# Kernel tuning notes

Measured on AMD Instinct MI355X. Metric: run time of the kernel, lower is better.

The kernel has to match this reference:

```python
import jax, jax.numpy as jnp
import numpy as np

N_NODES = 100000
N_EDGES = 1600000
IN_DIM = 128
HID_DIM = 32
OUT_DIM = 64
N_REL = 8
N_CLASSES = 2


def setup_inputs() -> dict:
    key = jax.random.key(0)
    ks = jax.random.split(key, 12)
    x = jax.random.normal(ks[0], (N_NODES, IN_DIM), dtype=jnp.float32)
    edge_index = jax.random.randint(ks[1], (2, N_EDGES), 0, N_NODES, dtype=jnp.int64)
    edge_type = jax.random.randint(ks[2], (N_EDGES,), 0, N_REL, dtype=jnp.int64)
    # FastRGCNConv params: per-relation weight W [R, in, out], root weight, bias
    def glorot(k, shape):
        fan_in, fan_out = shape[-2], shape[-1]
        s = jnp.sqrt(6.0 / (fan_in + fan_out))
        return jax.random.uniform(k, shape, jnp.float32, -s, s)
    W1 = glorot(ks[3], (N_REL, IN_DIM, HID_DIM))
    root1 = glorot(ks[4], (IN_DIM, HID_DIM))
    b1 = jnp.zeros((HID_DIM,), jnp.float32)
    W2 = glorot(ks[5], (N_REL, HID_DIM, OUT_DIM))
    root2 = glorot(ks[6], (HID_DIM, OUT_DIM))
    b2 = jnp.zeros((OUT_DIM,), jnp.float32)
    lin_w = glorot(ks[7], (OUT_DIM, N_CLASSES))
    lin_b = jnp.zeros((N_CLASSES,), jnp.float32)
    return {"x": x, "edge_index": edge_index, "edge_type": edge_type,
            "W1": W1, "root1": root1, "b1": b1,
            "W2": W2, "root2": root2, "b2": b2,
            "lin_w": lin_w, "lin_b": lin_b}


def _fast_rgcn_conv(x, W, root, b, src, dst, etype, n_nodes):
    """FastRGCNConv: per-relation transform, gather by (src, relation),
    mean-aggregate by destination, plus root transform and bias."""
    # Transform all nodes by all relation weights: [N, R, H]
    xW = jnp.einsum('nf,rfh->nrh', x, W)
    # Per-edge message: relation-specific transformed source feature [E, H]
    msg = xW[src, etype]
    agg = jax.ops.segment_sum(msg, dst, num_segments=n_nodes)
    deg = jax.ops.segment_sum(jnp.ones((src.shape[0],), x.dtype), dst,
                              num_segments=n_nodes)
    agg = agg / jnp.maximum(deg, 1.0)[:, None]  # mean aggregation
    return agg + x @ root + b


def reference(x, edge_index, edge_type, W1, root1, b1, W2, root2, b2, lin_w, lin_b):
    src, dst = edge_index[0], edge_index[1]
    n = x.shape[0]
    h = jax.nn.relu(_fast_rgcn_conv(x, W1, root1, b1, src, dst, edge_type, n))
    h = _fast_rgcn_conv(h, W2, root2, b2, src, dst, edge_type, n)
    return h @ lin_w + lin_b
```

## Files before the change

kernel.cpp:

```cpp
#include <hip/hip_runtime.h>

#define NN      100000
#define IN_DIM  128
#define HID     32
#define ODIM    64
#define L1C     288
#define L2K     288
#define NWGS    196
#define NCB     784
#define CCAP    40
#define RECCAP  2304
#define G2ST    296

using bf16x8 = __attribute__((ext_vector_type(8))) short;
using f32x4  = __attribute__((ext_vector_type(4))) float;

__device__ __forceinline__ float bf2f(short s) {
    unsigned int u = ((unsigned int)(unsigned short)s) << 16;
    float f; __builtin_memcpy(&f, &u, 4); return f;
}
__device__ __forceinline__ short f2bf(float f) {
    unsigned int u; __builtin_memcpy(&u, &f, 4);
    u += 0x7fffu + ((u >> 16) & 1u);
    return (short)(u >> 16);
}
__device__ __forceinline__ float ldf(const void* p, int i, int f32) {
    return f32 ? ((const float*)p)[i] : bf2f(((const short*)p)[i]);
}
__device__ __forceinline__ int ldi(const int* p, long long i, int i64) {
    return i64 ? p[2 * i] : p[(int)i];
}

__global__ __launch_bounds__(256) void detect(const short* __restrict__ x,
                                              const short* __restrict__ W1,
                                              const short* __restrict__ r1,
                                              const short* __restrict__ W2,
                                              const short* __restrict__ r2,
                                              const short* __restrict__ lw,
                                              const int* __restrict__ ei,
                                              const int* __restrict__ et,
                                              int* __restrict__ flags) {
    __shared__ int cnt[8];
    if (threadIdx.x < 8) cnt[threadIdx.x] = 0;
    __syncthreads();
    const short* ptrs[6] = {x, W1, r1, W2, r2, lw};
    const int    nsmp[6] = {2048, 2048, 2048, 2048, 1024, 64};
    for (int j = 0; j < 6; ++j) {
        int w = 0;
        for (int i = threadIdx.x; i < nsmp[j]; i += 256) {
            unsigned int s = (unsigned short)ptrs[j][2 * i];
            unsigned int e = (s >> 7) & 0xFF;
            if (e >= 140u || (e >= 1u && e <= 100u)) w++;
        }
        if (w) atomicAdd(&cnt[j], w);
    }
    int wi = 0, wt = 0;
    if (threadIdx.x < 128) {
        if (ei[2 * threadIdx.x + 1] != 0) wi = 1;
        if (et[2 * threadIdx.x + 1] != 0) wt = 1;
    }
    if (wi) atomicAdd(&cnt[6], 1);
    if (wt) atomicAdd(&cnt[7], 1);
    __syncthreads();
    if (threadIdx.x == 0) {
        const int ns[6] = {2048, 2048, 2048, 2048, 1024, 64};
        for (int j = 0; j < 6; ++j) flags[j] = (cnt[j] * 4 > ns[j]) ? 1 : 0;
        flags[6] = (cnt[6] == 0) ? 1 : 0;
        flags[7] = (cnt[7] == 0) ? 1 : 0;
    }
}

__global__ __launch_bounds__(256) void prep_w1(const void* __restrict__ W1,
                                               const void* __restrict__ root1,
                                               short* __restrict__ w1t,
                                               const int* __restrict__ flags) {
    int i = blockIdx.x * 256 + threadIdx.x;
    if (i >= L1C * IN_DIM) return;
    int c = i >> 7, f = i & 127;
    float v;
    if (c < 256) { int r = c >> 5, h = c & 31; v = ldf(W1, (r * IN_DIM + f) * HID + h, flags[1]); }
    else         { v = ldf(root1, f * HID + (c - 256), flags[2]); }
    w1t[c * IN_DIM + f] = f2bf(v);
}
__global__ __launch_bounds__(256) void prep_w2c(const void* __restrict__ W2,
                                                const void* __restrict__ root2,
                                                short* __restrict__ w2ct,
                                                const int* __restrict__ flags) {
    int i = blockIdx.x * 256 + threadIdx.x;
    if (i >= ODIM * L2K) return;
    int c = i / L2K, k = i % L2K;
    float v;
    if (k < 256) { int r = k >> 5, kk = k & 31; v = ldf(W2, (r * HID + kk) * ODIM + c, flags[3]); }
    else         { v = ldf(root2, (k - 256) * ODIM + c, flags[4]); }
    w2ct[c * L2K + k] = f2bf(v);
}
__global__ __launch_bounds__(256) void prep_small(const short* __restrict__ b1,
                                                  const short* __restrict__ b2,
                                                  const void* __restrict__ lin_w,
                                                  const short* __restrict__ lin_b,
                                                  short* __restrict__ smallc,
                                                  const int* __restrict__ flags) {
    int i = threadIdx.x;
    if (i < 32)        smallc[i] = b1[i];
    else if (i < 96)   smallc[i] = b2[i - 32];
    else if (i < 224)  smallc[i] = f2bf(ldf(lin_w, i - 96, flags[5]));
    else if (i < 226)  smallc[i] = lin_b[i - 224];
}

__global__ __launch_bounds__(1024) void scatter_coarse(const int* __restrict__ ei,
                                                       const int* __restrict__ et,
                                                       int* __restrict__ cnt,
                                                       int* __restrict__ seg, int E,
                                                       const int* __restrict__ flags) {
    __shared__ int cur[NCB];
    if (threadIdx.x < NCB) cur[threadIdx.x] = 0;
    __syncthreads();
    int i64 = flags[6], t64 = flags[7];
    int epw = (E + NWGS - 1) / NWGS;
    int lo = blockIdx.x * epw;
    int hi = lo + epw; if (hi > E) hi = E;
    for (int i = lo + threadIdx.x; i < hi; i += 1024) {
        int s = ldi(ei, i, i64);
        int d = ldi(ei, (long long)E + i, i64);
        int r = ldi(et, i, t64);
        int cb = d >> 7;
        int pos = atomicAdd(&cur[cb], 1);
        if (pos < CCAP)
            seg[(cb * NWGS + (int)blockIdx.x) * CCAP + pos] = ((d & 127) << 20) | (s << 3) | r;
    }
    __syncthreads();
    if (threadIdx.x < NCB) {
        int c = cur[threadIdx.x];
        cnt[blockIdx.x * NCB + threadIdx.x] = c < CCAP ? c : CCAP;
    }
}

__global__ __launch_bounds__(64) void cb_sum(const int* __restrict__ cnt,
                                             int* __restrict__ cbTot) {
    int cb = blockIdx.x, lane = threadIdx.x;
    int t = 0;
    for (int g = lane; g < NWGS; g += 64) t += cnt[g * NCB + cb];
#pragma unroll
    for (int o = 32; o > 0; o >>= 1) t += __shfl_down(t, o, 64);
    if (lane == 0) cbTot[cb] = t;
}

__global__ __launch_bounds__(1024) void cb_scan2(const int* __restrict__ cbTot,
                                                 int* __restrict__ cbBase,
                                                 int* __restrict__ off) {
    __shared__ int s[1024];
    int t = threadIdx.x;
    int v = (t < NCB) ? cbTot[t] : 0;
    s[t] = v; __syncthreads();
    for (int o = 1; o < 1024; o <<= 1) {
        int u = (t >= o) ? s[t - o] : 0;
        __syncthreads();
        s[t] += u;
        __syncthreads();
    }
    if (t < NCB) cbBase[t] = s[t] - v;
    if (t == NCB - 1) off[NN] = s[t];
}

__global__ __launch_bounds__(256) void build_cb(const int* __restrict__ cnt,
                                                const int* __restrict__ seg,
                                                const int* __restrict__ cbBase,
                                                int* __restrict__ off,
                                                float* __restrict__ inv_deg,
                                                int* __restrict__ packed) {
    __shared__ int cntl[NWGS], soff[NWGS];
    __shared__ int recs[RECCAP];
    __shared__ int degl[128], basel[128], kcur[128];
    __shared__ int stmp[256];
    int cb = blockIdx.x, tid = threadIdx.x;
    if (tid < NWGS) cntl[tid] = cnt[tid * NCB + cb];
    if (tid < 128) degl[tid] = 0;
    __syncthreads();
    int v = (tid < NWGS) ? cntl[tid] : 0;
    stmp[tid] = v; __syncthreads();
    for (int o = 1; o < 256; o <<= 1) {
        int u = (tid >= o) ? stmp[tid - o] : 0;
        __syncthreads();
        stmp[tid] += u;
        __syncthreads();
    }
    if (tid < NWGS) soff[tid] = stmp[tid] - v;
    int tot = stmp[255]; if (tot > RECCAP) tot = RECCAP;
    __syncthreads();
    int wave = tid >> 6, lane = tid & 63;
    for (int g = wave; g < NWGS; g += 4) {
        int c = cntl[g], b = soff[g];
        const int* sp = seg + (cb * NWGS + g) * CCAP;
        for (int e = lane; e < c; e += 64)
            if (b + e < RECCAP) recs[b + e] = sp[e];
    }
    __syncthreads();
    for (int i = tid; i < tot; i += 256) atomicAdd(&degl[recs[i] >> 20], 1);
    __syncthreads();
    int dv = (tid < 128) ? degl[tid] : 0;
    stmp[tid] = dv; __syncthreads();
    for (int o = 1; o < 128; o <<= 1) {
        int u = (tid >= o) ? stmp[tid - o] : 0;
        __syncthreads();
        stmp[tid] += u;
        __syncthreads();
    }
    int gbase = cbBase[cb];
    if (tid < 128) {
        int excl = stmp[tid] - dv;
        basel[tid] = excl;
        kcur[tid] = 0;
        int node = cb * 128 + tid;
        if (node < NN) {
            off[node] = gbase + excl;
            inv_deg[node] = 1.0f / (float)(dv > 1 ? dv : 1);
        }
    }
    __syncthreads();
    for (int i = tid; i < tot; i += 256) {
        int rec = recs[i];
        int n = rec >> 20;
        int p = atomicAdd(&kcur[n], 1);
        packed[gbase + basel[n] + p] = rec & 0xFFFFF;
    }
}

__global__ __launch_bounds__(256) void gemm1(const void* __restrict__ x,
                                             const short* __restrict__ w1t,
                                             short* __restrict__ xw,
                                             const int* __restrict__ flags) {
    int wave = threadIdx.x >> 6, lane = threadIdx.x & 63;
    int m = lane & 15, quad = lane >> 4;
    int row0 = (blockIdx.x * 4 + wave) * 64;
    if (row0 >= NN) return;

    bf16x8 a[4][4];
    int fp32 = flags[0];
#pragma unroll
    for (int t = 0; t < 4; ++t) {
        int row = row0 + t * 16 + m;
        int rc = row < NN ? row : NN - 1;
        if (fp32) {
            const float* xr = (const float*)x + rc * IN_DIM + quad * 8;
#pragma unroll
            for (int kt = 0; kt < 4; ++kt) {
                const f32x4* q = (const f32x4*)(xr + kt * 32);
                f32x4 u0 = q[0], u1 = q[1];
                bf16x8 tt;
                tt[0] = f2bf(u0[0]); tt[1] = f2bf(u0[1]); tt[2] = f2bf(u0[2]); tt[3] = f2bf(u0[3]);
                tt[4] = f2bf(u1[0]); tt[5] = f2bf(u1[1]); tt[6] = f2bf(u1[2]); tt[7] = f2bf(u1[3]);
                a[t][kt] = tt;
            }
        } else {
            const short* xr = (const short*)x + rc * IN_DIM + quad * 8;
#pragma unroll
            for (int kt = 0; kt < 4; ++kt) a[t][kt] = *(const bf16x8*)(xr + kt * 32);
        }
    }

    for (int ct = 0; ct < 18; ++ct) {
        const short* wp = w1t + (ct * 16 + m) * IN_DIM + quad * 8;
        bf16x8 b[4];
#pragma unroll
        for (int kt = 0; kt < 4; ++kt) b[kt] = *(const bf16x8*)(wp + kt * 32);
#pragma unroll
        for (int t = 0; t < 4; ++t) {
            f32x4 acc = {0.f, 0.f, 0.f, 0.f};
#pragma unroll
            for (int kt = 0; kt < 4; ++kt)
                acc = __builtin_amdgcn_mfma_f32_16x16x32_bf16(a[t][kt], b[kt], acc, 0, 0, 0);
#pragma unroll
            for (int i = 0; i < 4; ++i) {
                int r = row0 + t * 16 + quad * 4 + i;
                if (r < NN) xw[r * L1C + ct * 16 + m] = f2bf(acc[i]);
            }
        }
    }
}

__global__ __launch_bounds__(256) void agg1(const short* __restrict__ xw,
                                            const int* __restrict__ off,
                                            const int* __restrict__ packed,
                                            const float* __restrict__ inv_deg,
                                            const short* __restrict__ smallc,
                                            short* __restrict__ h) {
    int lane = threadIdx.x & 31;
    int node = blockIdx.x * 8 + (threadIdx.x >> 5);
    if (node >= NN) return;
    int s = off[node], e = off[node + 1];
    float acc = 0.f;
    int i = s;
    for (; i + 3 < e; i += 4) {
        int pk0 = packed[i], pk1 = packed[i + 1], pk2 = packed[i + 2], pk3 = packed[i + 3];
        float v0 = bf2f(xw[(pk0 >> 3) * L1C + (pk0 & 7) * 32 + lane]);
        float v1 = bf2f(xw[(pk1 >> 3) * L1C + (pk1 & 7) * 32 + lane]);
        float v2 = bf2f(xw[(pk2 >> 3) * L1C + (pk2 & 7) * 32 + lane]);
        float v3 = bf2f(xw[(pk3 >> 3) * L1C + (pk3 & 7) * 32 + lane]);
        acc += (v0 + v1) + (v2 + v3);
    }
    for (; i < e; ++i) {
        int pk = packed[i];
        acc += bf2f(xw[(pk >> 3) * L1C + (pk & 7) * 32 + lane]);
    }
    float v = acc * inv_deg[node] + bf2f(xw[node * L1C + 256 + lane]) + bf2f(smallc[lane]);
    h[node * HID + lane] = f2bf(v > 0.f ? v : 0.f);
}

__global__ __launch_bounds__(256) void agg2_fused(const short* __restrict__ h,
                                                  const int* __restrict__ off,
                                                  const int* __restrict__ packed,
                                                  const float* __restrict__ inv_deg,
                                                  const short* __restrict__ w2ct,
                                                  const short* __restrict__ smallc,
                                                  float* __restrict__ out) {
    __shared__ __align__(16) short g2l[16 * G2ST];
    __shared__ float red[4][16][2];
    int tid = threadIdx.x;
    int lane31 = tid & 31, gi = tid >> 5;
    int row0 = blockIdx.x * 16;

    for (int s2 = 0; s2 < 2; ++s2) {
        int n = row0 + gi * 2 + s2;
        int st = off[n], e = off[n + 1];
        float a0 = 0, a1 = 0, a2 = 0, a3 = 0, a4 = 0, a5 = 0, a6 = 0, a7 = 0;
        int i = st;
        for (; i + 3 < e; i += 4) {
            int pk0 = packed[i], pk1 = packed[i + 1], pk2 = packed[i + 2], pk3 = packed[i + 3];
            float v0 = bf2f(h[(pk0 >> 3) * HID + lane31]);
            float v1 = bf2f(h[(pk1 >> 3) * HID + lane31]);
            float v2 = bf2f(h[(pk2 >> 3) * HID + lane31]);
            float v3 = bf2f(h[(pk3 >> 3) * HID + lane31]);
            int r0 = pk0 & 7, r1 = pk1 & 7, r2 = pk2 & 7, r3 = pk3 & 7;
            a0 += ((r0 == 0) ? v0 : 0.f) + ((r1 == 0) ? v1 : 0.f) + ((r2 == 0) ? v2 : 0.f) + ((r3 == 0) ? v3 : 0.f);
            a1 += ((r0 == 1) ? v0 : 0.f) + ((r1 == 1) ? v1 : 0.f) + ((r2 == 1) ? v2 : 0.f) + ((r3 == 1) ? v3 : 0.f);
            a2 += ((r0 == 2) ? v0 : 0.f) + ((r1 == 2) ? v1 : 0.f) + ((r2 == 2) ? v2 : 0.f) + ((r3 == 2) ? v3 : 0.f);
            a3 += ((r0 == 3) ? v0 : 0.f) + ((r1 == 3) ? v1 : 0.f) + ((r2 == 3) ? v2 : 0.f) + ((r3 == 3) ? v3 : 0.f);
            a4 += ((r0 == 4) ? v0 : 0.f) + ((r1 == 4) ? v1 : 0.f) + ((r2 == 4) ? v2 : 0.f) + ((r3 == 4) ? v3 : 0.f);
            a5 += ((r0 == 5) ? v0 : 0.f) + ((r1 == 5) ? v1 : 0.f) + ((r2 == 5) ? v2 : 0.f) + ((r3 == 5) ? v3 : 0.f);
            a6 += ((r0 == 6) ? v0 : 0.f) + ((r1 == 6) ? v1 : 0.f) + ((r2 == 6) ? v2 : 0.f) + ((r3 == 6) ? v3 : 0.f);
            a7 += ((r0 == 7) ? v0 : 0.f) + ((r1 == 7) ? v1 : 0.f) + ((r2 == 7) ? v2 : 0.f) + ((r3 == 7) ? v3 : 0.f);
        }
        for (; i < e; ++i) {
            int pk = packed[i];
            float v = bf2f(h[(pk >> 3) * HID + lane31]);
            int r = pk & 7;
            a0 += (r == 0) ? v : 0.f;  a1 += (r == 1) ? v : 0.f;
            a2 += (r == 2) ? v : 0.f;  a3 += (r == 3) ? v : 0.f;
            a4 += (r == 4) ? v : 0.f;  a5 += (r == 5) ? v : 0.f;
            a6 += (r == 6) ? v : 0.f;  a7 += (r == 7) ? v : 0.f;
        }
        float sc = inv_deg[n];
        int base = (gi * 2 + s2) * G2ST;
        g2l[base +   0 + lane31] = f2bf(a0 * sc);
        g2l[base +  32 + lane31] = f2bf(a1 * sc);
        g2l[base +  64 + lane31] = f2bf(a2 * sc);
        g2l[base +  96 + lane31] = f2bf(a3 * sc);
        g2l[base + 128 + lane31] = f2bf(a4 * sc);
        g2l[base + 160 + lane31] = f2bf(a5 * sc);
        g2l[base + 192 + lane31] = f2bf(a6 * sc);
        g2l[base + 224 + lane31] = f2bf(a7 * sc);
        g2l[base + 256 + lane31] = h[n * HID + lane31];
    }
    __syncthreads();

    int wave = tid >> 6, lane = tid & 63;
    int m = lane & 15, quad = lane >> 4;
    const short* wp = w2ct + (wave * 16 + m) * L2K + quad * 8;
    bf16x8 a[9], b[9];
#pragma unroll
    for (int kt = 0; kt < 9; ++kt) {
        b[kt] = *(const bf16x8*)(wp + kt * 32);
        a[kt] = *(const bf16x8*)(&g2l[m * G2ST + quad * 8 + kt * 32]);
    }
    f32x4 acc = {0.f, 0.f, 0.f, 0.f};
#pragma unroll
    for (int kt = 0; kt < 9; ++kt)
        acc = __builtin_amdgcn_mfma_f32_16x16x32_bf16(a[kt], b[kt], acc, 0, 0, 0);

    int c = wave * 16 + m;
    float lw0 = bf2f(smallc[96 + c * 2 + 0]);
    float lw1 = bf2f(smallc[96 + c * 2 + 1]);
    float b2c = bf2f(smallc[32 + c]);
    float pr0[4], pr1[4];
#pragma unroll
    for (int i = 0; i < 4; ++i) {
        float v = acc[i] + b2c;
        pr0[i] = v * lw0;
        pr1[i] = v * lw1;
    }
#pragma unroll
    for (int o = 1; o < 16; o <<= 1) {
#pragma unroll
        for (int i = 0; i < 4; ++i) {
            pr0[i] += __shfl_xor(pr0[i], o, 64);
            pr1[i] += __shfl_xor(pr1[i], o, 64);
        }
    }
    if (m == 0) {
#pragma unroll
        for (int i = 0; i < 4; ++i) {
            red[wave][quad * 4 + i][0] = pr0[i];
            red[wave][quad * 4 + i][1] = pr1[i];
        }
    }
    __syncthreads();
    if (tid < 32) {
        int row = tid >> 1, j = tid & 1;
        float v = red[0][row][j] + red[1][row][j] + red[2][row][j] + red[3][row][j]
                + bf2f(smallc[224 + j]);
        out[(row0 + row) * 2 + j] = v;
    }
}

extern "C" void kernel_launch(void* const* d_in, const int* in_sizes, int n_in,
                              void* d_out, int out_size, void* d_ws, size_t ws_size,
                              hipStream_t stream) {
    const void* x     = d_in[0];
    const int*  ei    = (const int*)d_in[1];
    const int*  etype = (const int*)d_in[2];
    const void* W1    = d_in[3];
    const void* root1 = d_in[4];
    const void* b1    = d_in[5];
    const void* W2    = d_in[6];
    const void* root2 = d_in[7];
    const void* b2    = d_in[8];
    const void* lin_w = d_in[9];
    const void* lin_b = d_in[10];
    float* out = (float*)d_out;

    const int E = in_sizes[2];

    char* p = (char*)d_ws;
    auto alloc = [&](size_t bytes) { char* r = p; p += (bytes + 255) & ~(size_t)255; return (void*)r; };
    int*   flags   = (int*)  alloc(256);
    int*   off     = (int*)  alloc((size_t)(NN + 1) * 4);
    float* inv_deg = (float*)alloc((size_t)NN * 4);
    int*   packed  = (int*)  alloc((size_t)E * 4);
    int*   cnt     = (int*)  alloc((size_t)NWGS * NCB * 4);
    int*   cbTot   = (int*)  alloc((size_t)NCB * 4);
    int*   cbBase  = (int*)  alloc((size_t)NCB * 4);
    int*   seg     = (int*)  alloc((size_t)NCB * NWGS * CCAP * 4);
    short* w1t     = (short*)alloc((size_t)L1C * IN_DIM * 2);
    short* w2ct    = (short*)alloc((size_t)ODIM * L2K * 2);
    short* smallc  = (short*)alloc(256 * 2);
    short* h       = (short*)alloc((size_t)NN * HID * 2);
    short* xw1     = (short*)alloc((size_t)NN * L1C * 2);

    detect<<<1, 256, 0, stream>>>((const short*)x, (const short*)W1, (const short*)root1,
                                  (const short*)W2, (const short*)root2, (const short*)lin_w,
                                  ei, etype, flags);
    prep_w1<<<(L1C * IN_DIM + 255) / 256, 256, 0, stream>>>(W1, root1, w1t, flags);
    prep_w2c<<<(ODIM * L2K + 255) / 256, 256, 0, stream>>>(W2, root2, w2ct, flags);
    prep_small<<<1, 256, 0, stream>>>((const short*)b1, (const short*)b2, lin_w,
                                      (const short*)lin_b, smallc, flags);

    scatter_coarse<<<NWGS, 1024, 0, stream>>>(ei, etype, cnt, seg, E, flags);
    cb_sum<<<NCB, 64, 0, stream>>>(cnt, cbTot);
    cb_scan2<<<1, 1024, 0, stream>>>(cbTot, cbBase, off);
    build_cb<<<NCB, 256, 0, stream>>>(cnt, seg, cbBase, off, inv_deg, packed);

    gemm1<<<((NN + 63) / 64 + 3) / 4, 256, 0, stream>>>(x, w1t, xw1, flags);
    agg1<<<(NN + 7) / 8, 256, 0, stream>>>(xw1, off, packed, inv_deg, smallc, h);
    agg2_fused<<<NN / 16, 256, 0, stream>>>(h, off, packed, inv_deg, w2ct, smallc, out);
}
```

Measured before the change: 328.0 us.

## Recast layer-2 relation-binned aggregation as one-hot MFMA over edge chunks

Layer-2 aggregation previously had each 32-lane group loop over a node's edges and use eight select-accumulators, one per relation. It now processes the block's 16 nodes' contiguous edge range in chunks of 32. Gathered source features are transposed into LDS, a one-hot (node,relation) x edge matrix is built, and MFMA does the binning. The packed edge format gains the destination node's low 4 bits in bits 24+, and agg1 masks them off. This removes the per-edge compare/select arithmetic at the cost of three barriers per chunk, LDS zeroing, and mostly-zero MFMA work.

```diff
diff --git a/kernel.cpp b/kernel.cpp
--- a/kernel.cpp
+++ b/kernel.cpp
@@ -11,6 +11,8 @@
 #define CCAP    40
 #define RECCAP  2304
 #define G2ST    296
+#define PST     40
+#define HST     40
 
 using bf16x8 = __attribute__((ext_vector_type(8))) short;
 using f32x4  = __attribute__((ext_vector_type(4))) float;
@@ -221,7 +223,7 @@
         int rec = recs[i];
         int n = rec >> 20;
         int p = atomicAdd(&kcur[n], 1);
-        packed[gbase + basel[n] + p] = rec & 0xFFFFF;
+        packed[gbase + basel[n] + p] = ((n & 15) << 24) | (rec & 0xFFFFF);
     }
 }
 
@@ -292,15 +294,15 @@
     int i = s;
     for (; i + 3 < e; i += 4) {
         int pk0 = packed[i], pk1 = packed[i + 1], pk2 = packed[i + 2], pk3 = packed[i + 3];
-        float v0 = bf2f(xw[(pk0 >> 3) * L1C + (pk0 & 7) * 32 + lane]);
-        float v1 = bf2f(xw[(pk1 >> 3) * L1C + (pk1 & 7) * 32 + lane]);
-        float v2 = bf2f(xw[(pk2 >> 3) * L1C + (pk2 & 7) * 32 + lane]);
-        float v3 = bf2f(xw[(pk3 >> 3) * L1C + (pk3 & 7) * 32 + lane]);
+        float v0 = bf2f(xw[((pk0 >> 3) & 0x1FFFF) * L1C + (pk0 & 7) * 32 + lane]);
+        float v1 = bf2f(xw[((pk1 >> 3) & 0x1FFFF) * L1C + (pk1 & 7) * 32 + lane]);
+        float v2 = bf2f(xw[((pk2 >> 3) & 0x1FFFF) * L1C + (pk2 & 7) * 32 + lane]);
+        float v3 = bf2f(xw[((pk3 >> 3) & 0x1FFFF) * L1C + (pk3 & 7) * 32 + lane]);
         acc += (v0 + v1) + (v2 + v3);
     }
     for (; i < e; ++i) {
         int pk = packed[i];
-        acc += bf2f(xw[(pk >> 3) * L1C + (pk & 7) * 32 + lane]);
+        acc += bf2f(xw[((pk >> 3) & 0x1FFFF) * L1C + (pk & 7) * 32 + lane]);
     }
     float v = acc * inv_deg[node] + bf2f(xw[node * L1C + 256 + lane]) + bf2f(smallc[lane]);
     h[node * HID + lane] = f2bf(v > 0.f ? v : 0.f);
@@ -313,71 +315,91 @@
                                                   const short* __restrict__ w2ct,
                                                   const short* __restrict__ smallc,
                                                   float* __restrict__ out) {
+    __shared__ __align__(16) short Pl[128 * PST];
+    __shared__ __align__(16) short HgT[32 * HST];
     __shared__ __align__(16) short g2l[16 * G2ST];
     __shared__ float red[4][16][2];
+    __shared__ float invl[16];
     int tid = threadIdx.x;
-    int lane31 = tid & 31, gi = tid >> 5;
     int row0 = blockIdx.x * 16;
-
-    for (int s2 = 0; s2 < 2; ++s2) {
-        int n = row0 + gi * 2 + s2;
-        int st = off[n], e = off[n + 1];
-        float a0 = 0, a1 = 0, a2 = 0, a3 = 0, a4 = 0, a5 = 0, a6 = 0, a7 = 0;
-        int i = st;
-        for (; i + 3 < e; i += 4) {
-            int pk0 = packed[i], pk1 = packed[i + 1], pk2 = packed[i + 2], pk3 = packed[i + 3];
-            float v0 = bf2f(h[(pk0 >> 3) * HID + lane31]);
-            float v1 = bf2f(h[(pk1 >> 3) * HID + lane31]);
-            float v2 = bf2f(h[(pk2 >> 3) * HID + lane31]);
-            float v3 = bf2f(h[(pk3 >> 3) * HID + lane31]);
-            int r0 = pk0 & 7, r1 = pk1 & 7, r2 = pk2 & 7, r3 = pk3 & 7;
-            a0 += ((r0 == 0) ? v0 : 0.f) + ((r1 == 0) ? v1 : 0.f) + ((r2 == 0) ? v2 : 0.f) + ((r3 == 0) ? v3 : 0.f);
-            a1 += ((r0 == 1) ? v0 : 0.f) + ((r1 == 1) ? v1 : 0.f) + ((r2 == 1) ? v2 : 0.f) + ((r3 == 1) ? v3 : 0.f);
-            a2 += ((r0 == 2) ? v0 : 0.f) + ((r1 == 2) ? v1 : 0.f) + ((r2 == 2) ? v2 : 0.f) + ((r3 == 2) ? v3 : 0.f);
-            a3 += ((r0 == 3) ? v0 : 0.f) + ((r1 == 3) ? v1 : 0.f) + ((r2 == 3) ? v2 : 0.f) + ((r3 == 3) ? v3 : 0.f);
-            a4 += ((r0 == 4) ? v0 : 0.f) + ((r1 == 4) ? v1 : 0.f) + ((r2 == 4) ? v2 : 0.f) + ((r3 == 4) ? v3 : 0.f);
-            a5 += ((r0 == 5) ? v0 : 0.f) + ((r1 == 5) ? v1 : 0.f) + ((r2 == 5) ? v2 : 0.f) + ((r3 == 5) ? v3 : 0.f);
-            a6 += ((r0 == 6) ? v0 : 0.f) + ((r1 == 6) ? v1 : 0.f) + ((r2 == 6) ? v2 : 0.f) + ((r3 == 6) ? v3 : 0.f);
-            a7 += ((r0 == 7) ? v0 : 0.f) + ((r1 == 7) ? v1 : 0.f) + ((r2 == 7) ? v2 : 0.f) + ((r3 == 7) ? v3 : 0.f);
-        }
-        for (; i < e; ++i) {
-            int pk = packed[i];
-            float v = bf2f(h[(pk >> 3) * HID + lane31]);
-            int r = pk & 7;
-            a0 += (r == 0) ? v : 0.f;  a1 += (r == 1) ? v : 0.f;
-            a2 += (r == 2) ? v : 0.f;  a3 += (r == 3) ? v : 0.f;
-            a4 += (r == 4) ? v : 0.f;  a5 += (r == 5) ? v : 0.f;
-            a6 += (r == 6) ? v : 0.f;  a7 += (r == 7) ? v : 0.f;
-        }
-        float sc = inv_deg[n];
-        int base = (gi * 2 + s2) * G2ST;
-        g2l[base +   0 + lane31] = f2bf(a0 * sc);
-        g2l[base +  32 + lane31] = f2bf(a1 * sc);
-        g2l[base +  64 + lane31] = f2bf(a2 * sc);
-        g2l[base +  96 + lane31] = f2bf(a3 * sc);
-        g2l[base + 128 + lane31] = f2bf(a4 * sc);
-        g2l[base + 160 + lane31] = f2bf(a5 * sc);
-        g2l[base + 192 + lane31] = f2bf(a6 * sc);
-        g2l[base + 224 + lane31] = f2bf(a7 * sc);
-        g2l[base + 256 + lane31] = h[n * HID + lane31];
-    }
-    __syncthreads();
+    if (tid < 16) invl[tid] = inv_deg[row0 + tid];
+    int st = off[row0], en = off[row0 + 16];
 
     int wave = tid >> 6, lane = tid & 63;
-    int m = lane & 15, quad = lane >> 4;
-    const short* wp = w2ct + (wave * 16 + m) * L2K + quad * 8;
+    int m15 = lane & 15, quad = lane >> 4;
+    int e8 = tid >> 3;
+    int part = tid & 7;
+
+    f32x4 acc00 = {0,0,0,0}, acc01 = {0,0,0,0}, acc10 = {0,0,0,0}, acc11 = {0,0,0,0};
+
+    for (int c0 = st; c0 < en; c0 += 32) {
+        __syncthreads();
+        {
+            uint4 z = {0, 0, 0, 0};
+            uint4* pz = (uint4*)Pl;
+#pragma unroll
+            for (int j = 0; j < 2; ++j) pz[tid + j * 256] = z;
+            if (tid < 128) pz[tid + 512] = z;
+        }
+        int idx = c0 + e8;
+        int pk = (idx < en) ? packed[idx] : 0;
+        int src = (pk >> 3) & 0x1FFFF;
+        uint2 hv = *(const uint2*)(h + src * HID + part * 4);
+        short hs0 = (short)(hv.x & 0xFFFF), hs1 = (short)(hv.x >> 16);
+        short hs2 = (short)(hv.y & 0xFFFF), hs3 = (short)(hv.y >> 16);
+        HgT[(part * 4 + 0) * HST + e8] = hs0;
+        HgT[(part * 4 + 1) * HST + e8] = hs1;
+        HgT[(part * 4 + 2) * HST + e8] = hs2;
+        HgT[(part * 4 + 3) * HST + e8] = hs3;
+        __syncthreads();
+        if (part == 0 && idx < en) {
+            int row = ((pk >> 24) & 15) * 8 + (pk & 7);
+            Pl[row * PST + e8] = (short)0x3F80;
+        }
+        __syncthreads();
+        bf16x8 a0 = *(const bf16x8*)(&HgT[m15 * HST + quad * 8]);
+        bf16x8 a1 = *(const bf16x8*)(&HgT[(m15 + 16) * HST + quad * 8]);
+        bf16x8 b0 = *(const bf16x8*)(&Pl[((wave * 2 + 0) * 16 + m15) * PST + quad * 8]);
+        bf16x8 b1 = *(const bf16x8*)(&Pl[((wave * 2 + 1) * 16 + m15) * PST + quad * 8]);
+        acc00 = __builtin_amdgcn_mfma_f32_16x16x32_bf16(a0, b0, acc00, 0, 0, 0);
+        acc10 = __builtin_amdgcn_mfma_f32_16x16x32_bf16(a1, b0, acc10, 0, 0, 0);
+        acc01 = __builtin_amdgcn_mfma_f32_16x16x32_bf16(a0, b1, acc01, 0, 0, 0);
+        acc11 = __builtin_amdgcn_mfma_f32_16x16x32_bf16(a1, b1, acc11, 0, 0, 0);
+    }
+    __syncthreads();
+
+    {
+        int nr0 = (wave * 2 + 0) * 16 + m15;
+        int nr1 = (wave * 2 + 1) * 16 + m15;
+        float sc0 = invl[nr0 >> 3], sc1 = invl[nr1 >> 3];
+        int d0 = quad * 4;
+#pragma unroll
+        for (int i = 0; i < 4; ++i) {
+            g2l[(nr0 >> 3) * G2ST + (nr0 & 7) * 32 + d0 + i]      = f2bf(acc00[i] * sc0);
+            g2l[(nr0 >> 3) * G2ST + (nr0 & 7) * 32 + 16 + d0 + i] = f2bf(acc10[i] * sc0);
+            g2l[(nr1 >> 3) * G2ST + (nr1 & 7) * 32 + d0 + i]      = f2bf(acc01[i] * sc1);
+            g2l[(nr1 >> 3) * G2ST + (nr1 & 7) * 32 + 16 + d0 + i] = f2bf(acc11[i] * sc1);
+        }
+    }
+    for (int j = tid; j < 16 * 32; j += 256) {
+        int node = j >> 5, d = j & 31;
+        g2l[node * G2ST + 256 + d] = h[(row0 + node) * HID + d];
+    }
+    __syncthreads();
+
+    const short* wp = w2ct + (wave * 16 + m15) * L2K + quad * 8;
     bf16x8 a[9], b[9];
 #pragma unroll
     for (int kt = 0; kt < 9; ++kt) {
         b[kt] = *(const bf16x8*)(wp + kt * 32);
-        a[kt] = *(const bf16x8*)(&g2l[m * G2ST + quad * 8 + kt * 32]);
+        a[kt] = *(const bf16x8*)(&g2l[m15 * G2ST + quad * 8 + kt * 32]);
     }
     f32x4 acc = {0.f, 0.f, 0.f, 0.f};
 #pragma unroll
     for (int kt = 0; kt < 9; ++kt)
         acc = __builtin_amdgcn_mfma_f32_16x16x32_bf16(a[kt], b[kt], acc, 0, 0, 0);
 
-    int c = wave * 16 + m;
+    int c = wave * 16 + m15;
     float lw0 = bf2f(smallc[96 + c * 2 + 0]);
     float lw1 = bf2f(smallc[96 + c * 2 + 1]);
     float b2c = bf2f(smallc[32 + c]);
@@ -396,7 +418,7 @@
             pr1[i] += __shfl_xor(pr1[i], o, 64);
         }
     }
-    if (m == 0) {
+    if (m15 == 0) {
 #pragma unroll
         for (int i = 0; i < 4; ++i) {
             red[wave][quad * 4 + i][0] = pr0[i];
```

Result: slower. 338.1 us (+3.1%).
